# Performance work log

Measured on AMD Instinct MI355X. Metric: run time of the kernel, lower is better.

Reference implementation:

```python
import jax, jax.numpy as jnp
import numpy as np

B, IMG, P, S, D, H, HD = 64, 224, 16, 197, 768, 12, 64
MLP, L, PRUNE_AFTER, NCLS = 3072, 12, 4, 1000
N_KEEP = max(1, int(S * 0.5))  # FIXED_RATIO = 0.5 -> 98 kept tokens (plus forced CLS)


def _ln(x, w, b, eps=1e-6):
    m = x.mean(-1, keepdims=True)
    v = ((x - m) ** 2).mean(-1, keepdims=True)
    return (x - m) * jax.lax.rsqrt(v + eps) * w + b


def _block(x, ln1_w, ln1_b, qkv_w, qkv_b, proj_w, proj_b,
           ln2_w, ln2_b, fc1_w, fc1_b, fc2_w, fc2_b, key_mask=None):
    b, s, _ = x.shape
    qkv = _ln(x, ln1_w, ln1_b) @ qkv_w.T + qkv_b           # [B,S,3D]
    qkv = qkv.reshape(b, s, 3, H, HD)
    q, k, v = qkv[:, :, 0], qkv[:, :, 1], qkv[:, :, 2]     # [B,S,H,HD]
    logits = jnp.einsum('bqhd,bkhd->bhqk', q * (HD ** -0.5), k)
    if key_mask is not None:
        # masking pruned keys == varlen attention restricted to kept tokens
        logits = jnp.where(key_mask[:, None, None, :], logits, -1e9)
    attn = jax.nn.softmax(logits, axis=-1)
    out = jnp.einsum('bhqk,bkhd->bqhd', attn, v).reshape(b, s, D)
    x = x + out @ proj_w.T + proj_b
    h = _ln(x, ln2_w, ln2_b)
    h = jax.nn.gelu(h @ fc1_w.T + fc1_b, approximate=False) @ fc2_w.T + fc2_b
    return x + h


def _forward(images, patch_w, patch_b, cls_token, pos_embed,
             ln1_w, ln1_b, qkv_w, qkv_b, proj_w, proj_b,
             ln2_w, ln2_b, fc1_w, fc1_b, fc2_w, fc2_b,
             norm_w, norm_b, head_w, head_b):
    # patch embed: conv stride P == non-overlapping patch projection
    x = jax.lax.conv_general_dilated(images, patch_w, (P, P), 'VALID',
                                     dimension_numbers=('NCHW', 'OIHW', 'NCHW'))
    x = x.reshape(x.shape[0], D, -1).transpose(0, 2, 1) + patch_b       # [B,196,D]
    x = jnp.concatenate([jnp.broadcast_to(cls_token, (x.shape[0], 1, D)), x], axis=1)
    x = x + pos_embed                                                    # [B,197,D]
    for i in range(PRUNE_AFTER):
        x = _block(x, ln1_w[i], ln1_b[i], qkv_w[i], qkv_b[i], proj_w[i], proj_b[i],
                   ln2_w[i], ln2_b[i], fc1_w[i], fc1_b[i], fc2_w[i], fc2_b[i])
    # norm-score topk prune (CLS always kept), as in _threshold_prune
    scores = jnp.linalg.norm(x, axis=-1)                                 # [B,S]
    _, idx = jax.lax.top_k(scores, N_KEEP)
    mask = jnp.zeros((x.shape[0], S), bool)
    mask = mask.at[jnp.arange(x.shape[0])[:, None], idx].set(True).at[:, 0].set(True)
    # Padded-mask form of triton_pack_tokens + flash_attn_varlen: pruned tokens
    # are never attended to (masked keys) and their own outputs are unused.
    for i in range(PRUNE_AFTER, L):
        x = _block(x, ln1_w[i], ln1_b[i], qkv_w[i], qkv_b[i], proj_w[i], proj_b[i],
                   ln2_w[i], ln2_b[i], fc1_w[i], fc1_b[i], fc2_w[i], fc2_b[i],
                   key_mask=mask)
    cls = _ln(x[:, 0], norm_w, norm_b)   # packed[cu[:-1]] is always the CLS token
    return cls @ head_w.T + head_b       # [B, NCLS]


def setup_inputs():
    key = jax.random.key(0)
    ks = iter(jax.random.split(key, 32))
    def rn(shape, s=0.02):
        return jax.random.normal(next(ks), shape, jnp.float32) * s
    return {
        'images': jax.random.normal(next(ks), (B, 3, IMG, IMG), jnp.float32),
        'patch_w': rn((D, 3, P, P)), 'patch_b': jnp.zeros((D,), jnp.float32),
        'cls_token': rn((1, 1, D)), 'pos_embed': rn((1, S, D)),
        'ln1_w': jnp.ones((L, D), jnp.float32), 'ln1_b': jnp.zeros((L, D), jnp.float32),
        'qkv_w': rn((L, 3 * D, D)), 'qkv_b': jnp.zeros((L, 3 * D), jnp.float32),
        'proj_w': rn((L, D, D)), 'proj_b': jnp.zeros((L, D), jnp.float32),
        'ln2_w': jnp.ones((L, D), jnp.float32), 'ln2_b': jnp.zeros((L, D), jnp.float32),
        'fc1_w': rn((L, MLP, D)), 'fc1_b': jnp.zeros((L, MLP), jnp.float32),
        'fc2_w': rn((L, D, MLP)), 'fc2_b': jnp.zeros((L, D), jnp.float32),
        'norm_w': jnp.ones((D,), jnp.float32), 'norm_b': jnp.zeros((D,), jnp.float32),
        'head_w': rn((NCLS, D)), 'head_b': jnp.zeros((NCLS,), jnp.float32),
    }


def reference(images, patch_w, patch_b, cls_token, pos_embed,
              ln1_w, ln1_b, qkv_w, qkv_b, proj_w, proj_b,
              ln2_w, ln2_b, fc1_w, fc1_b, fc2_w, fc2_b,
              norm_w, norm_b, head_w, head_b):
    return _forward(images, patch_w, patch_b, cls_token, pos_embed,
                    ln1_w, ln1_b, qkv_w, qkv_b, proj_w, proj_b,
                    ln2_w, ln2_b, fc1_w, fc1_b, fc2_w, fc2_b,
                    norm_w, norm_b, head_w, head_b)
```

## Files before the change

kernel.cpp:

```cpp
#include <hip/hip_runtime.h>
#include <hip/hip_bf16.h>
#include <cstdint>

#define NH 12
#define SQ 197
#define DIM 768
#define HDIM 64
#define BATCH 64
#define MTOK (BATCH*SQ)
#define MLPD 3072
#define NKEEP 98
#define CSLOT 100
#define MCTOK (BATCH*CSLOT)
#define VLDF 224
#define VLDC 128

typedef __attribute__((ext_vector_type(8))) short bf16x8;
typedef __attribute__((ext_vector_type(8))) unsigned short ushort8;
typedef __attribute__((ext_vector_type(4))) float floatx4;

__device__ __forceinline__ unsigned short f2bf(float f) {
  __hip_bfloat16 h = __float2bfloat16(f);
  return reinterpret_cast<unsigned short&>(h);
}

__device__ __forceinline__ float erf_fast(float x) {
  float ax = fabsf(x);
  float t = 1.f / (1.f + 0.3275911f * ax);
  float y = t * (0.254829592f + t * (-0.284496736f + t * (1.421413741f +
            t * (-1.453152027f + t * 1.061405429f))));
  float r = 1.f - y * __expf(-ax * ax);
  return copysignf(r, x);
}

__device__ __forceinline__ void gload16(const unsigned short* g, unsigned short* l) {
  __builtin_amdgcn_global_load_lds(
      (const __attribute__((address_space(1))) void*)g,
      (__attribute__((address_space(3))) void*)l, 16, 0, 0);
}

enum { EPI_PATCH = 0, EPI_QKV = 1, EPI_RESID = 2, EPI_GELU = 3, EPI_HEAD = 4, EPI_QKVC = 5 };

template<int EPI, bool CHK>
__device__ __forceinline__ void gemm_epilogue(
    floatx4 (&acc)[4][4], int m0, int n0, int wr, int wc, int l15, int l4,
    const float* __restrict__ bias, int M, int N,
    float* __restrict__ xresid, const float* __restrict__ pos,
    unsigned short* __restrict__ obf, unsigned short* __restrict__ qb,
    unsigned short* __restrict__ kb, unsigned short* __restrict__ vb,
    float* __restrict__ ofp)
{
#pragma unroll
  for (int mr = 0; mr < 4; ++mr) {
#pragma unroll
    for (int nr = 0; nr < 4; ++nr) {
#pragma unroll
      for (int j = 0; j < 4; ++j) {
        int m = m0 + wr + mr * 16 + l4 * 4 + j;
        int n = n0 + wc + nr * 16 + l15;
        if (CHK && (m >= M || n >= N)) continue;
        float val = acc[mr][nr][j] + bias[n];
        if constexpr (EPI == EPI_PATCH) {
          int b = m / 196, p = m - b * 196;
          xresid[(size_t)(b * SQ + 1 + p) * DIM + n] = val + pos[(1 + p) * DIM + n];
        } else if constexpr (EPI == EPI_QKV || EPI == EPI_QKVC) {
          constexpr int SR = (EPI == EPI_QKV) ? SQ : CSLOT;
          constexpr int VL = (EPI == EPI_QKV) ? VLDF : VLDC;
          int part = n / DIM; int within = n - part * DIM;
          int h = within >> 6, hd = within & 63;
          int b = m / SR, s = m - b * SR;
          if (part == 0)      qb[(((size_t)(b * NH + h)) * SR + s) * HDIM + hd] = f2bf(val * 0.125f);
          else if (part == 1) kb[(((size_t)(b * NH + h)) * SR + s) * HDIM + hd] = f2bf(val);
          else                vb[(((size_t)(b * NH + h)) * HDIM + hd) * VL + s] = f2bf(val);
        } else if constexpr (EPI == EPI_RESID) {
          xresid[(size_t)m * DIM + n] += val;
        } else if constexpr (EPI == EPI_GELU) {
          float g = 0.5f * val * (1.f + erf_fast(val * 0.70710678118654752f));
          obf[(size_t)m * MLPD + n] = f2bf(g);
        } else {
          ofp[(size_t)m * 1000 + n] = val;
        }
      }
    }
  }
}

template<int EPI>
__global__ __launch_bounds__(256)
void gemm_bf(const unsigned short* __restrict__ A, int lda,
             const unsigned short* __restrict__ Wb, int ldw,
             const float* __restrict__ bias,
             int M, int N, int K,
             float* __restrict__ xresid,
             const float* __restrict__ pos,
             unsigned short* __restrict__ obf,
             unsigned short* __restrict__ qb,
             unsigned short* __restrict__ kb,
             unsigned short* __restrict__ vb,
             float* __restrict__ ofp)
{
  __shared__ unsigned short As[128 * 64];
  __shared__ unsigned short Bs[128 * 64];
  const int tid = threadIdx.x;
  const int lane = tid & 63;
  const int w = tid >> 6;
  const int wr = (w >> 1) * 64, wc = (w & 1) * 64;
  const int m0 = blockIdx.y * 128, n0 = blockIdx.x * 128;
  const int l15 = lane & 15, l4 = lane >> 4;

  const int sub = lane & 7, rsub = lane >> 3;
  const int scol = ((sub ^ rsub) << 3);
  const unsigned short* gA[4];
  const unsigned short* gB[4];
  unsigned short* lA[4];
  unsigned short* lB[4];
#pragma unroll
  for (int j = 0; j < 4; ++j) {
    int t = w * 4 + j;
    int row = t * 8 + rsub;
    int ra = m0 + row; if (ra > M - 1) ra = M - 1;
    int rb = n0 + row; if (rb > N - 1) rb = N - 1;
    gA[j] = A + (size_t)ra * lda + scol;
    gB[j] = Wb + (size_t)rb * ldw + scol;
    lA[j] = &As[t * 512];
    lB[j] = &Bs[t * 512];
  }

  floatx4 acc[4][4];
#pragma unroll
  for (int i = 0; i < 4; ++i)
#pragma unroll
    for (int j = 0; j < 4; ++j) acc[i][j] = {0.f, 0.f, 0.f, 0.f};

  for (int kt = 0; kt < K; kt += 64) {
#pragma unroll
    for (int j = 0; j < 4; ++j) {
      gload16(gA[j] + kt, lA[j]);
      gload16(gB[j] + kt, lB[j]);
    }
    __syncthreads();
#pragma unroll
    for (int kk = 0; kk < 2; ++kk) {
      bf16x8 af[4], bfr[4];
#pragma unroll
      for (int mr = 0; mr < 4; ++mr) {
        int row = wr + mr * 16 + l15;
        int cs = (kk * 4 + l4) ^ (row & 7);
        af[mr] = *(const bf16x8*)&As[row * 64 + cs * 8];
      }
#pragma unroll
      for (int nr = 0; nr < 4; ++nr) {
        int row = wc + nr * 16 + l15;
        int cs = (kk * 4 + l4) ^ (row & 7);
        bfr[nr] = *(const bf16x8*)&Bs[row * 64 + cs * 8];
      }
#pragma unroll
      for (int mr = 0; mr < 4; ++mr)
#pragma unroll
        for (int nr = 0; nr < 4; ++nr)
          acc[mr][nr] = __builtin_amdgcn_mfma_f32_16x16x32_bf16(af[mr], bfr[nr], acc[mr][nr], 0, 0, 0);
    }
    __syncthreads();
  }
  if (m0 + 128 <= M && n0 + 128 <= N)
    gemm_epilogue<EPI, false>(acc, m0, n0, wr, wc, l15, l4, bias, M, N,
                              xresid, pos, obf, qb, kb, vb, ofp);
  else
    gemm_epilogue<EPI, true>(acc, m0, n0, wr, wc, l15, l4, bias, M, N,
                             xresid, pos, obf, qb, kb, vb, ofp);
}

template<int EPI>
__global__ __launch_bounds__(256)
void gemm_f32(const unsigned short* __restrict__ A, int lda,
              const float* __restrict__ Wf, int ldw,
              const float* __restrict__ bias,
              int M, int N, int K,
              float* __restrict__ xresid,
              const float* __restrict__ pos,
              unsigned short* __restrict__ obf,
              unsigned short* __restrict__ qb,
              unsigned short* __restrict__ kb,
              unsigned short* __restrict__ vb,
              float* __restrict__ ofp)
{
  __shared__ unsigned short As[128 * 64];
  __shared__ unsigned short Bs[128 * 64];
  const int tid = threadIdx.x;
  const int lane = tid & 63;
  const int w = tid >> 6;
  const int wr = (w >> 1) * 64, wc = (w & 1) * 64;
  const int m0 = blockIdx.y * 128, n0 = blockIdx.x * 128;
  const int l15 = lane & 15, l4 = lane >> 4;

  floatx4 acc[4][4];
#pragma unroll
  for (int i = 0; i < 4; ++i)
#pragma unroll
    for (int j = 0; j < 4; ++j) acc[i][j] = {0.f, 0.f, 0.f, 0.f};

  for (int kt = 0; kt < K; kt += 64) {
#pragma unroll
    for (int i = 0; i < 4; ++i) {
      int g = tid + 256 * i;
      int row = g >> 3, c = g & 7;
      int sw = (c ^ (row & 7)) * 8;
      int ra = m0 + row; if (ra > M - 1) ra = M - 1;
      ushort8 av = *(const ushort8*)(A + (size_t)ra * lda + kt + c * 8);
      *(ushort8*)&As[row * 64 + sw] = av;
      int rb = n0 + row; if (rb > N - 1) rb = N - 1;
      const float* bs = Wf + (size_t)rb * ldw + kt + c * 8;
      float4 f0 = *(const float4*)bs;
      float4 f1 = *(const float4*)(bs + 4);
      ushort8 bv;
      bv[0] = f2bf(f0.x); bv[1] = f2bf(f0.y); bv[2] = f2bf(f0.z); bv[3] = f2bf(f0.w);
      bv[4] = f2bf(f1.x); bv[5] = f2bf(f1.y); bv[6] = f2bf(f1.z); bv[7] = f2bf(f1.w);
      *(ushort8*)&Bs[row * 64 + sw] = bv;
    }
    __syncthreads();
#pragma unroll
    for (int kk = 0; kk < 2; ++kk) {
      bf16x8 af[4], bfr[4];
#pragma unroll
      for (int mr = 0; mr < 4; ++mr) {
        int row = wr + mr * 16 + l15;
        int cs = (kk * 4 + l4) ^ (row & 7);
        af[mr] = *(const bf16x8*)&As[row * 64 + cs * 8];
      }
#pragma unroll
      for (int nr = 0; nr < 4; ++nr) {
        int row = wc + nr * 16 + l15;
        int cs = (kk * 4 + l4) ^ (row & 7);
        bfr[nr] = *(const bf16x8*)&Bs[row * 64 + cs * 8];
      }
#pragma unroll
      for (int mr = 0; mr < 4; ++mr)
#pragma unroll
        for (int nr = 0; nr < 4; ++nr)
          acc[mr][nr] = __builtin_amdgcn_mfma_f32_16x16x32_bf16(af[mr], bfr[nr], acc[mr][nr], 0, 0, 0);
    }
    __syncthreads();
  }
  if (m0 + 128 <= M && n0 + 128 <= N)
    gemm_epilogue<EPI, false>(acc, m0, n0, wr, wc, l15, l4, bias, M, N,
                              xresid, pos, obf, qb, kb, vb, ofp);
  else
    gemm_epilogue<EPI, true>(acc, m0, n0, wr, wc, l15, l4, bias, M, N,
                             xresid, pos, obf, qb, kb, vb, ofp);
}

__global__ __launch_bounds__(256)
void cvt_kernel(const float* __restrict__ src, unsigned short* __restrict__ dst, int nchunks)
{
  int i = blockIdx.x * 256 + threadIdx.x;
  if (i >= nchunks) return;
  float4 f0 = *(const float4*)(src + (size_t)i * 8);
  float4 f1 = *(const float4*)(src + (size_t)i * 8 + 4);
  ushort8 v;
  v[0] = f2bf(f0.x); v[1] = f2bf(f0.y); v[2] = f2bf(f0.z); v[3] = f2bf(f0.w);
  v[4] = f2bf(f1.x); v[5] = f2bf(f1.y); v[6] = f2bf(f1.z); v[7] = f2bf(f1.w);
  *(ushort8*)(dst + (size_t)i * 8) = v;
}

__global__ __launch_bounds__(256)
void ln_kernel(const float* __restrict__ x, long long row_stride,
               const float* __restrict__ g, const float* __restrict__ b,
               unsigned short* __restrict__ out)
{
  int row = blockIdx.x;
  const float* xr = x + (size_t)row * row_stride;
  int t = threadIdx.x;
  float v0 = xr[t], v1 = xr[t + 256], v2 = xr[t + 512];
  float s = v0 + v1 + v2, sq = v0 * v0 + v1 * v1 + v2 * v2;
  __shared__ float sb[8];
  for (int o = 32; o; o >>= 1) { s += __shfl_down(s, o); sq += __shfl_down(sq, o); }
  if ((t & 63) == 0) { sb[t >> 6] = s; sb[4 + (t >> 6)] = sq; }
  __syncthreads();
  s = sb[0] + sb[1] + sb[2] + sb[3];
  sq = sb[4] + sb[5] + sb[6] + sb[7];
  float mean = s * (1.f / 768.f);
  float var = sq * (1.f / 768.f) - mean * mean;
  float rstd = rsqrtf(var + 1e-6f);
  unsigned short* orow = out + (size_t)row * DIM;
  orow[t]       = f2bf((v0 - mean) * rstd * g[t]       + b[t]);
  orow[t + 256] = f2bf((v1 - mean) * rstd * g[t + 256] + b[t + 256]);
  orow[t + 512] = f2bf((v2 - mean) * rstd * g[t + 512] + b[t + 512]);
}

template<int NT, int SROWS, int VLD, int PSTR, bool CNT>
__global__ __launch_bounds__(256)
void attn_kernel(const unsigned short* __restrict__ qb,
                 const unsigned short* __restrict__ kb,
                 const unsigned short* __restrict__ vb,
                 const int* __restrict__ cnt,
                 unsigned short* __restrict__ outA)
{
  __shared__ unsigned short Ks[NT * 16 * 64];
  __shared__ unsigned short Ps[4][16 * PSTR];
  int bh = blockIdx.x;
  int b = bh / NH, h = bh - b * NH;
  const int tid = threadIdx.x, lane = tid & 63, w = tid >> 6;
  const int l15 = lane & 15, l4 = lane >> 4;
  const unsigned short* kbase = kb + (size_t)bh * SROWS * HDIM;
  const unsigned short* qbase = qb + (size_t)bh * SROWS * HDIM;
  const unsigned short* vbase = vb + (size_t)bh * HDIM * VLD;
  const int limit = CNT ? cnt[b] : SROWS;

  constexpr int KCH = NT * 16 * 8;
  for (int i = 0; i < (KCH + 255) / 256; ++i) {
    int gch = tid + 256 * i;
    if (gch < KCH) {
      int row = gch >> 3, c = gch & 7;
      int rs = row > SROWS - 1 ? SROWS - 1 : row;
      ushort8 kv = *(const ushort8*)(kbase + (size_t)rs * HDIM + c * 8);
      *(ushort8*)&Ks[row * 64 + ((c ^ (row & 7))) * 8] = kv;
    }
  }
  __syncthreads();

  for (int qt = w; qt < NT; qt += 4) {
    int qrow = qt * 16 + l15; if (qrow > SROWS - 1) qrow = SROWS - 1;
    bf16x8 aq0 = *(const bf16x8*)(qbase + (size_t)qrow * HDIM + l4 * 8);
    bf16x8 aq1 = *(const bf16x8*)(qbase + (size_t)qrow * HDIM + 32 + l4 * 8);

    floatx4 lg[NT];
#pragma unroll
    for (int nt = 0; nt < NT; ++nt) {
      lg[nt] = {0.f, 0.f, 0.f, 0.f};
      int row = nt * 16 + l15;
      int cs0 = (l4) ^ (row & 7);
      int cs1 = (4 + l4) ^ (row & 7);
      bf16x8 bk0 = *(const bf16x8*)&Ks[row * 64 + cs0 * 8];
      bf16x8 bk1 = *(const bf16x8*)&Ks[row * 64 + cs1 * 8];
      lg[nt] = __builtin_amdgcn_mfma_f32_16x16x32_bf16(aq0, bk0, lg[nt], 0, 0, 0);
      lg[nt] = __builtin_amdgcn_mfma_f32_16x16x32_bf16(aq1, bk1, lg[nt], 0, 0, 0);
    }
    float mx[4] = {-1e30f, -1e30f, -1e30f, -1e30f};
#pragma unroll
    for (int nt = 0; nt < NT; ++nt) {
      int col = nt * 16 + l15;
      bool valid = col < limit;
#pragma unroll
      for (int j = 0; j < 4; ++j) {
        float v = valid ? lg[nt][j] : -1e9f;
        lg[nt][j] = v;
        mx[j] = fmaxf(mx[j], v);
      }
    }
#pragma unroll
    for (int j = 0; j < 4; ++j)
      for (int o = 1; o < 16; o <<= 1) mx[j] = fmaxf(mx[j], __shfl_xor(mx[j], o));
    float sm[4] = {0.f, 0.f, 0.f, 0.f};
#pragma unroll
    for (int nt = 0; nt < NT; ++nt)
#pragma unroll
      for (int j = 0; j < 4; ++j) {
        float p = __expf(lg[nt][j] - mx[j]);
        lg[nt][j] = p;
        sm[j] += p;
      }
#pragma unroll
    for (int j = 0; j < 4; ++j) {
      for (int o = 1; o < 16; o <<= 1) sm[j] += __shfl_xor(sm[j], o);
      sm[j] = 1.f / sm[j];
    }
    unsigned short* pw = &Ps[w][0];
#pragma unroll
    for (int nt = 0; nt < NT; ++nt) {
      int col = nt * 16 + l15;
#pragma unroll
      for (int j = 0; j < 4; ++j)
        pw[(l4 * 4 + j) * PSTR + col] = f2bf(lg[nt][j]);
    }
#pragma unroll
    for (int j = 0; j < 4; ++j)
      pw[(l4 * 4 + j) * PSTR + NT * 16 + l15] = 0;
    floatx4 oacc[4];
#pragma unroll
    for (int nr = 0; nr < 4; ++nr) oacc[nr] = {0.f, 0.f, 0.f, 0.f};
#pragma unroll
    for (int ks = 0; ks < VLD / 32; ++ks) {
      bf16x8 ap = *(const bf16x8*)&pw[l15 * PSTR + ks * 32 + l4 * 8];
#pragma unroll
      for (int nr = 0; nr < 4; ++nr) {
        bf16x8 bv = *(const bf16x8*)(vbase + (size_t)(nr * 16 + l15) * VLD + ks * 32 + l4 * 8);
        oacc[nr] = __builtin_amdgcn_mfma_f32_16x16x32_bf16(ap, bv, oacc[nr], 0, 0, 0);
      }
    }
#pragma unroll
    for (int nr = 0; nr < 4; ++nr)
#pragma unroll
      for (int j = 0; j < 4; ++j) {
        int qi = qt * 16 + l4 * 4 + j;
        if (qi < SROWS)
          outA[((size_t)(b * SROWS + qi)) * DIM + h * HDIM + nr * 16 + l15] = f2bf(oacc[nr][j] * sm[j]);
      }
  }
}

__global__ __launch_bounds__(256)
void im2col_kernel(const float* __restrict__ images, unsigned short* __restrict__ out)
{
  int idx = blockIdx.x * 256 + threadIdx.x;
  int token = idx / 96;
  int kc = (idx - token * 96) * 8;
  int b = token / 196, p = token - b * 196;
  int py = p / 14, px = p - py * 14;
  int c = kc >> 8, rem = kc & 255;
  int i = rem >> 4, j0 = rem & 15;
  const float* src = images + (((size_t)(b * 3 + c) * 224 + py * 16 + i) * 224 + px * 16 + j0);
  float4 f0 = *(const float4*)src;
  float4 f1 = *(const float4*)(src + 4);
  ushort8 v;
  v[0] = f2bf(f0.x); v[1] = f2bf(f0.y); v[2] = f2bf(f0.z); v[3] = f2bf(f0.w);
  v[4] = f2bf(f1.x); v[5] = f2bf(f1.y); v[6] = f2bf(f1.z); v[7] = f2bf(f1.w);
  *(ushort8*)(out + (size_t)token * DIM + kc) = v;
}

__global__ __launch_bounds__(256)
void clspos_kernel(const float* __restrict__ cls, const float* __restrict__ pos,
                   float* __restrict__ x)
{
  int idx = blockIdx.x * 256 + threadIdx.x;
  int b = idx / DIM, d = idx - b * DIM;
  x[(size_t)(b * SQ) * DIM + d] = cls[d] + pos[d];
}

__global__ __launch_bounds__(256)
void norms_kernel(const float* __restrict__ x, float* __restrict__ norms)
{
  int row = blockIdx.x * 4 + (threadIdx.x >> 6);
  if (row >= MTOK) return;
  int lane = threadIdx.x & 63;
  const float* xr = x + (size_t)row * DIM;
  float acc = 0.f;
  for (int d = lane; d < DIM; d += 64) { float v = xr[d]; acc += v * v; }
  for (int o = 32; o; o >>= 1) acc += __shfl_down(acc, o);
  if (lane == 0) norms[row] = acc;
}

__global__ __launch_bounds__(256)
void topk_select(const float* __restrict__ norms, short* __restrict__ sidx,
                 int* __restrict__ cntg)
{
  int b = blockIdx.x;
  __shared__ float sc[SQ];
  __shared__ unsigned char keep[SQ];
  int tid = threadIdx.x;
  if (tid < SQ) sc[tid] = norms[b * SQ + tid];
  __syncthreads();
  if (tid < SQ) {
    float mine = sc[tid];
    int rank = 0;
    for (int j = 0; j < SQ; ++j) {
      float v = sc[j];
      rank += (v > mine) || (v == mine && j < tid);
    }
    keep[tid] = (rank < NKEEP) || (tid == 0);
  }
  __syncthreads();
  if (tid == 0) {
    short* row = sidx + b * CSLOT;
    int c = 0;
    for (int s = 0; s < SQ; ++s) if (keep[s]) row[c++] = (short)s;
    cntg[b] = c;
    for (int s = c; s < CSLOT; ++s) row[s] = 0;
  }
}

__global__ __launch_bounds__(192)
void gather_kernel(const float* __restrict__ x, const short* __restrict__ sidx,
                   float* __restrict__ xc)
{
  int g = blockIdx.x;
  int b = g / CSLOT;
  int src = sidx[g];
  const float4* sp = (const float4*)(x + ((size_t)(b * SQ + src)) * DIM);
  float4* dp = (float4*)(xc + (size_t)g * DIM);
  dp[threadIdx.x] = sp[threadIdx.x];
}

template<int EPI>
static inline void launch_gemm(dim3 grid, hipStream_t stream, bool usebf,
                               const unsigned short* A, int lda,
                               const float* Wf, const unsigned short* Wb, int ldw,
                               const float* bias, int M, int N, int K,
                               float* xresid, const float* pos,
                               unsigned short* obf, unsigned short* qb,
                               unsigned short* kb, unsigned short* vb, float* ofp)
{
  if (usebf)
    gemm_bf<EPI><<<grid, 256, 0, stream>>>(A, lda, Wb, ldw, bias,
        M, N, K, xresid, pos, obf, qb, kb, vb, ofp);
  else
    gemm_f32<EPI><<<grid, 256, 0, stream>>>(A, lda, Wf, ldw, bias,
        M, N, K, xresid, pos, obf, qb, kb, vb, ofp);
}

extern "C" void kernel_launch(void* const* d_in, const int* in_sizes, int n_in,
                              void* d_out, int out_size, void* d_ws, size_t ws_size,
                              hipStream_t stream)
{
  const float* images    = (const float*)d_in[0];
  const float* patch_w   = (const float*)d_in[1];
  const float* patch_b   = (const float*)d_in[2];
  const float* cls_token = (const float*)d_in[3];
  const float* pos_embed = (const float*)d_in[4];
  const float* ln1_w = (const float*)d_in[5];
  const float* ln1_b = (const float*)d_in[6];
  const float* qkv_w = (const float*)d_in[7];
  const float* qkv_b = (const float*)d_in[8];
  const float* proj_w = (const float*)d_in[9];
  const float* proj_b = (const float*)d_in[10];
  const float* ln2_w = (const float*)d_in[11];
  const float* ln2_b = (const float*)d_in[12];
  const float* fc1_w = (const float*)d_in[13];
  const float* fc1_b = (const float*)d_in[14];
  const float* fc2_w = (const float*)d_in[15];
  const float* fc2_b = (const float*)d_in[16];
  const float* norm_w = (const float*)d_in[17];
  const float* norm_b = (const float*)d_in[18];
  const float* head_w = (const float*)d_in[19];
  const float* head_b = (const float*)d_in[20];

  char* ws = (char*)d_ws;
  size_t off = 0;
  auto alloc = [&](size_t bytes) { void* p = ws + off; off += (bytes + 255) & ~(size_t)255; return p; };
  float* x            = (float*)alloc((size_t)MTOK * DIM * 4);
  float* xc           = (float*)alloc((size_t)MCTOK * DIM * 4);
  unsigned short* xn  = (unsigned short*)alloc((size_t)MTOK * DIM * 2);
  size_t h1_bytes = (size_t)MTOK * MLPD * 2;
  unsigned short* h1  = (unsigned short*)alloc(h1_bytes);
  unsigned short* qb  = h1;
  unsigned short* kb  = qb + (size_t)BATCH * NH * SQ * HDIM;
  unsigned short* vb  = kb + (size_t)BATCH * NH * SQ * HDIM;
  size_t vbytes = (size_t)BATCH * NH * HDIM * VLDF * 2;
  unsigned short* lncls = (unsigned short*)alloc((size_t)64 * DIM * 2);
  float* norms = (float*)alloc((size_t)MTOK * 4);
  short* sidx  = (short*)alloc((size_t)MCTOK * 2);
  int* cnt = (int*)alloc(BATCH * 4);
  size_t n_qkvw = (size_t)12 * 2304 * DIM, n_projw = (size_t)12 * DIM * DIM;
  size_t n_fc1w = (size_t)12 * MLPD * DIM, n_fc2w = (size_t)12 * DIM * MLPD;
  size_t n_patw = (size_t)DIM * DIM, n_headw = (size_t)1000 * DIM;
  unsigned short* wqkv = (unsigned short*)alloc(n_qkvw * 2);
  unsigned short* wproj = (unsigned short*)alloc(n_projw * 2);
  unsigned short* wfc1 = (unsigned short*)alloc(n_fc1w * 2);
  unsigned short* wfc2 = (unsigned short*)alloc(n_fc2w * 2);
  unsigned short* wpat = (unsigned short*)alloc(n_patw * 2);
  unsigned short* whead = (unsigned short*)alloc(n_headw * 2);
  const bool usebf = (off <= ws_size);

  hipMemsetAsync(vb, 0, vbytes, stream);

  if (usebf) {
    cvt_kernel<<<(int)((n_qkvw/8 + 255)/256), 256, 0, stream>>>(qkv_w, wqkv, (int)(n_qkvw/8));
    cvt_kernel<<<(int)((n_projw/8 + 255)/256), 256, 0, stream>>>(proj_w, wproj, (int)(n_projw/8));
    cvt_kernel<<<(int)((n_fc1w/8 + 255)/256), 256, 0, stream>>>(fc1_w, wfc1, (int)(n_fc1w/8));
    cvt_kernel<<<(int)((n_fc2w/8 + 255)/256), 256, 0, stream>>>(fc2_w, wfc2, (int)(n_fc2w/8));
    cvt_kernel<<<(int)((n_patw/8 + 255)/256), 256, 0, stream>>>(patch_w, wpat, (int)(n_patw/8));
    cvt_kernel<<<(int)((n_headw/8 + 255)/256), 256, 0, stream>>>(head_w, whead, (int)(n_headw/8));
  }

  im2col_kernel<<<4704, 256, 0, stream>>>(images, h1);
  launch_gemm<EPI_PATCH>(dim3(6, 98), stream, usebf, h1, DIM, patch_w, wpat, DIM,
      patch_b, 12544, DIM, DIM, x, pos_embed, nullptr, nullptr, nullptr, nullptr, nullptr);
  clspos_kernel<<<192, 256, 0, stream>>>(cls_token, pos_embed, x);

  for (int l = 0; l < 4; ++l) {
    ln_kernel<<<MTOK, 256, 0, stream>>>(x, DIM, ln1_w + l * DIM, ln1_b + l * DIM, xn);
    launch_gemm<EPI_QKV>(dim3(18, 99), stream, usebf, xn, DIM,
        qkv_w + (size_t)l * 2304 * DIM, wqkv + (size_t)l * 2304 * DIM, DIM,
        qkv_b + l * 2304, MTOK, 2304, DIM, nullptr, nullptr, nullptr, qb, kb, vb, nullptr);
    attn_kernel<13, SQ, VLDF, 248, false><<<BATCH * NH, 256, 0, stream>>>(qb, kb, vb, nullptr, xn);
    launch_gemm<EPI_RESID>(dim3(6, 99), stream, usebf, xn, DIM,
        proj_w + (size_t)l * DIM * DIM, wproj + (size_t)l * DIM * DIM, DIM,
        proj_b + l * DIM, MTOK, DIM, DIM, x, nullptr, nullptr, nullptr, nullptr, nullptr, nullptr);
    ln_kernel<<<MTOK, 256, 0, stream>>>(x, DIM, ln2_w + l * DIM, ln2_b + l * DIM, xn);
    launch_gemm<EPI_GELU>(dim3(24, 99), stream, usebf, xn, DIM,
        fc1_w + (size_t)l * MLPD * DIM, wfc1 + (size_t)l * MLPD * DIM, DIM,
        fc1_b + l * MLPD, MTOK, MLPD, DIM, nullptr, nullptr, h1, nullptr, nullptr, nullptr, nullptr);
    launch_gemm<EPI_RESID>(dim3(6, 99), stream, usebf, h1, MLPD,
        fc2_w + (size_t)l * DIM * MLPD, wfc2 + (size_t)l * DIM * MLPD, MLPD,
        fc2_b + l * DIM, MTOK, DIM, MLPD, x, nullptr, nullptr, nullptr, nullptr, nullptr, nullptr);
  }

  norms_kernel<<<(MTOK + 3) / 4, 256, 0, stream>>>(x, norms);
  topk_select<<<BATCH, 256, 0, stream>>>(norms, sidx, cnt);
  gather_kernel<<<MCTOK, 192, 0, stream>>>(x, sidx, xc);

  for (int l = 4; l < 12; ++l) {
    ln_kernel<<<MCTOK, 256, 0, stream>>>(xc, DIM, ln1_w + l * DIM, ln1_b + l * DIM, xn);
    launch_gemm<EPI_QKVC>(dim3(18, 50), stream, usebf, xn, DIM,
        qkv_w + (size_t)l * 2304 * DIM, wqkv + (size_t)l * 2304 * DIM, DIM,
        qkv_b + l * 2304, MCTOK, 2304, DIM, nullptr, nullptr, nullptr, qb, kb, vb, nullptr);
    attn_kernel<7, CSLOT, VLDC, 136, true><<<BATCH * NH, 256, 0, stream>>>(qb, kb, vb, cnt, xn);
    launch_gemm<EPI_RESID>(dim3(6, 50), stream, usebf, xn, DIM,
        proj_w + (size_t)l * DIM * DIM, wproj + (size_t)l * DIM * DIM, DIM,
        proj_b + l * DIM, MCTOK, DIM, DIM, xc, nullptr, nullptr, nullptr, nullptr, nullptr, nullptr);
    ln_kernel<<<MCTOK, 256, 0, stream>>>(xc, DIM, ln2_w + l * DIM, ln2_b + l * DIM, xn);
    launch_gemm<EPI_GELU>(dim3(24, 50), stream, usebf, xn, DIM,
        fc1_w + (size_t)l * MLPD * DIM, wfc1 + (size_t)l * MLPD * DIM, DIM,
        fc1_b + l * MLPD, MCTOK, MLPD, DIM, nullptr, nullptr, h1, nullptr, nullptr, nullptr, nullptr);
    launch_gemm<EPI_RESID>(dim3(6, 50), stream, usebf, h1, MLPD,
        fc2_w + (size_t)l * DIM * MLPD, wfc2 + (size_t)l * DIM * MLPD, MLPD,
        fc2_b + l * DIM, MCTOK, DIM, MLPD, xc, nullptr, nullptr, nullptr, nullptr, nullptr, nullptr);
  }

  ln_kernel<<<64, 256, 0, stream>>>(xc, (long long)CSLOT * DIM, norm_w, norm_b, lncls);
  launch_gemm<EPI_HEAD>(dim3(8, 1), stream, usebf, lncls, DIM, head_w, whead, DIM,
      head_b, 64, 1000, DIM, nullptr, nullptr, nullptr, nullptr, nullptr, nullptr, (float*)d_out);
  (void)in_sizes; (void)n_in; (void)out_size;
}
```

Measured before the change: 4.114 ms.

## Double-buffer LDS tiles in bf16 GEMM and remap workgroups across XCDs

New measurement: 3.848 ms. -6.5%, faster.

```diff
diff --git a/kernel.cpp b/kernel.cpp
--- a/kernel.cpp
+++ b/kernel.cpp
@@ -99,21 +99,27 @@
              unsigned short* __restrict__ vb,
              float* __restrict__ ofp)
 {
-  __shared__ unsigned short As[128 * 64];
-  __shared__ unsigned short Bs[128 * 64];
+  __shared__ unsigned short As[2][128 * 64];
+  __shared__ unsigned short Bs[2][128 * 64];
   const int tid = threadIdx.x;
   const int lane = tid & 63;
   const int w = tid >> 6;
   const int wr = (w >> 1) * 64, wc = (w & 1) * 64;
-  const int m0 = blockIdx.y * 128, n0 = blockIdx.x * 128;
+
+  const int gx = gridDim.x;
+  const int nwg = gx * gridDim.y;
+  const int orig = blockIdx.y * gx + blockIdx.x;
+  const int q = nwg >> 3, r = nwg & 7;
+  const int xcd = orig & 7, o8 = orig >> 3;
+  const int wgid = ((xcd < r) ? xcd * (q + 1) : r * (q + 1) + (xcd - r) * q) + o8;
+  const int bx = wgid % gx, by = wgid / gx;
+  const int m0 = by * 128, n0 = bx * 128;
   const int l15 = lane & 15, l4 = lane >> 4;
 
   const int sub = lane & 7, rsub = lane >> 3;
   const int scol = ((sub ^ rsub) << 3);
   const unsigned short* gA[4];
   const unsigned short* gB[4];
-  unsigned short* lA[4];
-  unsigned short* lB[4];
 #pragma unroll
   for (int j = 0; j < 4; ++j) {
     int t = w * 4 + j;
@@ -122,9 +128,18 @@
     int rb = n0 + row; if (rb > N - 1) rb = N - 1;
     gA[j] = A + (size_t)ra * lda + scol;
     gB[j] = Wb + (size_t)rb * ldw + scol;
-    lA[j] = &As[t * 512];
-    lB[j] = &Bs[t * 512];
-  }
+  }
+
+  auto STAGE = [&](int buf, int kt) {
+    unsigned short* Ad = &As[buf][0];
+    unsigned short* Bd = &Bs[buf][0];
+#pragma unroll
+    for (int j = 0; j < 4; ++j) {
+      int t = w * 4 + j;
+      gload16(gA[j] + kt, Ad + t * 512);
+      gload16(gB[j] + kt, Bd + t * 512);
+    }
+  };
 
   floatx4 acc[4][4];
 #pragma unroll
@@ -132,13 +147,20 @@
 #pragma unroll
     for (int j = 0; j < 4; ++j) acc[i][j] = {0.f, 0.f, 0.f, 0.f};
 
-  for (int kt = 0; kt < K; kt += 64) {
-#pragma unroll
-    for (int j = 0; j < 4; ++j) {
-      gload16(gA[j] + kt, lA[j]);
-      gload16(gB[j] + kt, lB[j]);
-    }
-    __syncthreads();
+  const int nk = K >> 6;
+  STAGE(0, 0);
+  int cur = 0;
+  for (int ki = 0; ki < nk; ++ki) {
+    if (ki + 1 < nk) {
+      STAGE(cur ^ 1, (ki + 1) << 6);
+      asm volatile("s_waitcnt vmcnt(8)" ::: "memory");
+    } else {
+      asm volatile("s_waitcnt vmcnt(0)" ::: "memory");
+    }
+    __builtin_amdgcn_sched_barrier(0);
+    __builtin_amdgcn_s_barrier();
+    const unsigned short* Ac = &As[cur][0];
+    const unsigned short* Bc = &Bs[cur][0];
 #pragma unroll
     for (int kk = 0; kk < 2; ++kk) {
       bf16x8 af[4], bfr[4];
@@ -146,13 +168,13 @@
       for (int mr = 0; mr < 4; ++mr) {
         int row = wr + mr * 16 + l15;
         int cs = (kk * 4 + l4) ^ (row & 7);
-        af[mr] = *(const bf16x8*)&As[row * 64 + cs * 8];
+        af[mr] = *(const bf16x8*)&Ac[row * 64 + cs * 8];
       }
 #pragma unroll
       for (int nr = 0; nr < 4; ++nr) {
         int row = wc + nr * 16 + l15;
         int cs = (kk * 4 + l4) ^ (row & 7);
-        bfr[nr] = *(const bf16x8*)&Bs[row * 64 + cs * 8];
+        bfr[nr] = *(const bf16x8*)&Bc[row * 64 + cs * 8];
       }
 #pragma unroll
       for (int mr = 0; mr < 4; ++mr)
@@ -160,7 +182,9 @@
         for (int nr = 0; nr < 4; ++nr)
           acc[mr][nr] = __builtin_amdgcn_mfma_f32_16x16x32_bf16(af[mr], bfr[nr], acc[mr][nr], 0, 0, 0);
     }
-    __syncthreads();
+    __builtin_amdgcn_sched_barrier(0);
+    __builtin_amdgcn_s_barrier();
+    cur ^= 1;
   }
   if (m0 + 128 <= M && n0 + 128 <= N)
     gemm_epilogue<EPI, false>(acc, m0, n0, wr, wc, l15, l4, bias, M, N,
```

## Add BN-templated GEMM tiles and XCD-aware workgroup remapping

Applied to the files above, without the earlier changes.

Measured after the change: 3.715 ms. -9.7%, faster.

```diff
diff --git a/kernel.cpp b/kernel.cpp
--- a/kernel.cpp
+++ b/kernel.cpp
@@ -41,9 +41,9 @@
 
 enum { EPI_PATCH = 0, EPI_QKV = 1, EPI_RESID = 2, EPI_GELU = 3, EPI_HEAD = 4, EPI_QKVC = 5 };
 
-template<int EPI, bool CHK>
+template<int EPI, bool CHK, int NR>
 __device__ __forceinline__ void gemm_epilogue(
-    floatx4 (&acc)[4][4], int m0, int n0, int wr, int wc, int l15, int l4,
+    floatx4 (&acc)[4][NR], int m0, int n0, int wr, int wc, int l15, int l4,
     const float* __restrict__ bias, int M, int N,
     float* __restrict__ xresid, const float* __restrict__ pos,
     unsigned short* __restrict__ obf, unsigned short* __restrict__ qb,
@@ -53,7 +53,7 @@
 #pragma unroll
   for (int mr = 0; mr < 4; ++mr) {
 #pragma unroll
-    for (int nr = 0; nr < 4; ++nr) {
+    for (int nr = 0; nr < NR; ++nr) {
 #pragma unroll
       for (int j = 0; j < 4; ++j) {
         int m = m0 + wr + mr * 16 + l4 * 4 + j;
@@ -85,7 +85,7 @@
   }
 }
 
-template<int EPI>
+template<int EPI, int BN>
 __global__ __launch_bounds__(256)
 void gemm_bf(const unsigned short* __restrict__ A, int lda,
              const unsigned short* __restrict__ Wb, int ldw,
@@ -99,49 +99,61 @@
              unsigned short* __restrict__ vb,
              float* __restrict__ ofp)
 {
+  constexpr int NR = BN / 32;
+  constexpr int NG = (128 + BN) / 8;
+  constexpr int PG = NG / 4;
   __shared__ unsigned short As[128 * 64];
-  __shared__ unsigned short Bs[128 * 64];
+  __shared__ unsigned short Bs[BN * 64];
   const int tid = threadIdx.x;
   const int lane = tid & 63;
   const int w = tid >> 6;
-  const int wr = (w >> 1) * 64, wc = (w & 1) * 64;
-  const int m0 = blockIdx.y * 128, n0 = blockIdx.x * 128;
+  const int wr = (w >> 1) * 64, wc = (w & 1) * (BN / 2);
+
+  const int gx = gridDim.x;
+  const int nwg = gx * gridDim.y;
+  const int orig = blockIdx.y * gx + blockIdx.x;
+  const int q = nwg >> 3, r = nwg & 7;
+  const int xcd = orig & 7, o8 = orig >> 3;
+  const int wgid = ((xcd < r) ? xcd * (q + 1) : r * (q + 1) + (xcd - r) * q) + o8;
+  const int bx = wgid % gx, by = wgid / gx;
+  const int m0 = by * 128, n0 = bx * BN;
   const int l15 = lane & 15, l4 = lane >> 4;
 
   const int sub = lane & 7, rsub = lane >> 3;
   const int scol = ((sub ^ rsub) << 3);
-  const unsigned short* gA[4];
-  const unsigned short* gB[4];
-  unsigned short* lA[4];
-  unsigned short* lB[4];
-#pragma unroll
-  for (int j = 0; j < 4; ++j) {
-    int t = w * 4 + j;
-    int row = t * 8 + rsub;
-    int ra = m0 + row; if (ra > M - 1) ra = M - 1;
-    int rb = n0 + row; if (rb > N - 1) rb = N - 1;
-    gA[j] = A + (size_t)ra * lda + scol;
-    gB[j] = Wb + (size_t)rb * ldw + scol;
-    lA[j] = &As[t * 512];
-    lB[j] = &Bs[t * 512];
-  }
-
-  floatx4 acc[4][4];
+  const unsigned short* gp[PG];
+  unsigned short* lp[PG];
+#pragma unroll
+  for (int j = 0; j < PG; ++j) {
+    int t = w * PG + j;
+    if (t < 16) {
+      int row = t * 8 + rsub;
+      int ra = m0 + row; if (ra > M - 1) ra = M - 1;
+      gp[j] = A + (size_t)ra * lda + scol;
+      lp[j] = &As[t * 512];
+    } else {
+      int tb = t - 16;
+      int row = tb * 8 + rsub;
+      int rb = n0 + row; if (rb > N - 1) rb = N - 1;
+      gp[j] = Wb + (size_t)rb * ldw + scol;
+      lp[j] = &Bs[tb * 512];
+    }
+  }
+
+  floatx4 acc[4][NR];
 #pragma unroll
   for (int i = 0; i < 4; ++i)
 #pragma unroll
-    for (int j = 0; j < 4; ++j) acc[i][j] = {0.f, 0.f, 0.f, 0.f};
+    for (int j = 0; j < NR; ++j) acc[i][j] = {0.f, 0.f, 0.f, 0.f};
 
   for (int kt = 0; kt < K; kt += 64) {
 #pragma unroll
-    for (int j = 0; j < 4; ++j) {
-      gload16(gA[j] + kt, lA[j]);
-      gload16(gB[j] + kt, lB[j]);
-    }
+    for (int j = 0; j < PG; ++j)
+      gload16(gp[j] + kt, lp[j]);
     __syncthreads();
 #pragma unroll
     for (int kk = 0; kk < 2; ++kk) {
-      bf16x8 af[4], bfr[4];
+      bf16x8 af[4], bfr[NR];
 #pragma unroll
       for (int mr = 0; mr < 4; ++mr) {
         int row = wr + mr * 16 + l15;
@@ -149,7 +161,7 @@
         af[mr] = *(const bf16x8*)&As[row * 64 + cs * 8];
       }
 #pragma unroll
-      for (int nr = 0; nr < 4; ++nr) {
+      for (int nr = 0; nr < NR; ++nr) {
         int row = wc + nr * 16 + l15;
         int cs = (kk * 4 + l4) ^ (row & 7);
         bfr[nr] = *(const bf16x8*)&Bs[row * 64 + cs * 8];
@@ -157,17 +169,17 @@
 #pragma unroll
       for (int mr = 0; mr < 4; ++mr)
 #pragma unroll
-        for (int nr = 0; nr < 4; ++nr)
+        for (int nr = 0; nr < NR; ++nr)
           acc[mr][nr] = __builtin_amdgcn_mfma_f32_16x16x32_bf16(af[mr], bfr[nr], acc[mr][nr], 0, 0, 0);
     }
     __syncthreads();
   }
-  if (m0 + 128 <= M && n0 + 128 <= N)
-    gemm_epilogue<EPI, false>(acc, m0, n0, wr, wc, l15, l4, bias, M, N,
-                              xresid, pos, obf, qb, kb, vb, ofp);
+  if (m0 + 128 <= M && n0 + BN <= N)
+    gemm_epilogue<EPI, false, NR>(acc, m0, n0, wr, wc, l15, l4, bias, M, N,
+                                  xresid, pos, obf, qb, kb, vb, ofp);
   else
-    gemm_epilogue<EPI, true>(acc, m0, n0, wr, wc, l15, l4, bias, M, N,
-                             xresid, pos, obf, qb, kb, vb, ofp);
+    gemm_epilogue<EPI, true, NR>(acc, m0, n0, wr, wc, l15, l4, bias, M, N,
+                                 xresid, pos, obf, qb, kb, vb, ofp);
 }
 
 template<int EPI>
@@ -242,11 +254,11 @@
     __syncthreads();
   }
   if (m0 + 128 <= M && n0 + 128 <= N)
-    gemm_epilogue<EPI, false>(acc, m0, n0, wr, wc, l15, l4, bias, M, N,
-                              xresid, pos, obf, qb, kb, vb, ofp);
+    gemm_epilogue<EPI, false, 4>(acc, m0, n0, wr, wc, l15, l4, bias, M, N,
+                                 xresid, pos, obf, qb, kb, vb, ofp);
   else
-    gemm_epilogue<EPI, true>(acc, m0, n0, wr, wc, l15, l4, bias, M, N,
-                             xresid, pos, obf, qb, kb, vb, ofp);
+    gemm_epilogue<EPI, true, 4>(acc, m0, n0, wr, wc, l15, l4, bias, M, N,
+                                xresid, pos, obf, qb, kb, vb, ofp);
 }
 
 __global__ __launch_bounds__(256)
@@ -480,8 +492,8 @@
   dp[threadIdx.x] = sp[threadIdx.x];
 }
 
-template<int EPI>
-static inline void launch_gemm(dim3 grid, hipStream_t stream, bool usebf,
+template<int EPI, int BN>
+static inline void launch_gemm(hipStream_t stream, bool usebf,
                                const unsigned short* A, int lda,
                                const float* Wf, const unsigned short* Wb, int ldw,
                                const float* bias, int M, int N, int K,
@@ -489,12 +501,15 @@
                                unsigned short* obf, unsigned short* qb,
                                unsigned short* kb, unsigned short* vb, float* ofp)
 {
-  if (usebf)
-    gemm_bf<EPI><<<grid, 256, 0, stream>>>(A, lda, Wb, ldw, bias,
+  if (usebf) {
+    dim3 grid((N + BN - 1) / BN, (M + 127) / 128);
+    gemm_bf<EPI, BN><<<grid, 256, 0, stream>>>(A, lda, Wb, ldw, bias,
         M, N, K, xresid, pos, obf, qb, kb, vb, ofp);
-  else
+  } else {
+    dim3 grid((N + 127) / 128, (M + 127) / 128);
     gemm_f32<EPI><<<grid, 256, 0, stream>>>(A, lda, Wf, ldw, bias,
         M, N, K, xresid, pos, obf, qb, kb, vb, ofp);
+  }
 }
 
 extern "C" void kernel_launch(void* const* d_in, const int* in_sizes, int n_in,
@@ -562,24 +577,24 @@
   }
 
   im2col_kernel<<<4704, 256, 0, stream>>>(images, h1);
-  launch_gemm<EPI_PATCH>(dim3(6, 98), stream, usebf, h1, DIM, patch_w, wpat, DIM,
+  launch_gemm<EPI_PATCH, 64>(stream, usebf, h1, DIM, patch_w, wpat, DIM,
       patch_b, 12544, DIM, DIM, x, pos_embed, nullptr, nullptr, nullptr, nullptr, nullptr);
   clspos_kernel<<<192, 256, 0, stream>>>(cls_token, pos_embed, x);
 
   for (int l = 0; l < 4; ++l) {
     ln_kernel<<<MTOK, 256, 0, stream>>>(x, DIM, ln1_w + l * DIM, ln1_b + l * DIM, xn);
-    launch_gemm<EPI_QKV>(dim3(18, 99), stream, usebf, xn, DIM,
+    launch_gemm<EPI_QKV, 128>(stream, usebf, xn, DIM,
         qkv_w + (size_t)l * 2304 * DIM, wqkv + (size_t)l * 2304 * DIM, DIM,
         qkv_b + l * 2304, MTOK, 2304, DIM, nullptr, nullptr, nullptr, qb, kb, vb, nullptr);
     attn_kernel<13, SQ, VLDF, 248, false><<<BATCH * NH, 256, 0, stream>>>(qb, kb, vb, nullptr, xn);
-    launch_gemm<EPI_RESID>(dim3(6, 99), stream, usebf, xn, DIM,
+    launch_gemm<EPI_RESID, 64>(stream, usebf, xn, DIM,
         proj_w + (size_t)l * DIM * DIM, wproj + (size_t)l * DIM * DIM, DIM,
         proj_b + l * DIM, MTOK, DIM, DIM, x, nullptr, nullptr, nullptr, nullptr, nullptr, nullptr);
     ln_kernel<<<MTOK, 256, 0, stream>>>(x, DIM, ln2_w + l * DIM, ln2_b + l * DIM, xn);
-    launch_gemm<EPI_GELU>(dim3(24, 99), stream, usebf, xn, DIM,
+    launch_gemm<EPI_GELU, 128>(stream, usebf, xn, DIM,
         fc1_w + (size_t)l * MLPD * DIM, wfc1 + (size_t)l * MLPD * DIM, DIM,
         fc1_b + l * MLPD, MTOK, MLPD, DIM, nullptr, nullptr, h1, nullptr, nullptr, nullptr, nullptr);
-    launch_gemm<EPI_RESID>(dim3(6, 99), stream, usebf, h1, MLPD,
+    launch_gemm<EPI_RESID, 64>(stream, usebf, h1, MLPD,
         fc2_w + (size_t)l * DIM * MLPD, wfc2 + (size_t)l * DIM * MLPD, MLPD,
         fc2_b + l * DIM, MTOK, DIM, MLPD, x, nullptr, nullptr, nullptr, nullptr, nullptr, nullptr);
   }
@@ -590,24 +605,24 @@
 
   for (int l = 4; l < 12; ++l) {
     ln_kernel<<<MCTOK, 256, 0, stream>>>(xc, DIM, ln1_w + l * DIM, ln1_b + l * DIM, xn);
-    launch_gemm<EPI_QKVC>(dim3(18, 50), stream, usebf, xn, DIM,
+    launch_gemm<EPI_QKVC, 128>(stream, usebf, xn, DIM,
         qkv_w + (size_t)l * 2304 * DIM, wqkv + (size_t)l * 2304 * DIM, DIM,
         qkv_b + l * 2304, MCTOK, 2304, DIM, nullptr, nullptr, nullptr, qb, kb, vb, nullptr);
     attn_kernel<7, CSLOT, VLDC, 136, true><<<BATCH * NH, 256, 0, stream>>>(qb, kb, vb, cnt, xn);
-    launch_gemm<EPI_RESID>(dim3(6, 50), stream, usebf, xn, DIM,
+    launch_gemm<EPI_RESID, 64>(stream, usebf, xn, DIM,
         proj_w + (size_t)l * DIM * DIM, wproj + (size_t)l * DIM * DIM, DIM,
         proj_b + l * DIM, MCTOK, DIM, DIM, xc, nullptr, nullptr, nullptr, nullptr, nullptr, nullptr);
     ln_kernel<<<MCTOK, 256, 0, stream>>>(xc, DIM, ln2_w + l * DIM, ln2_b + l * DIM, xn);
-    launch_gemm<EPI_GELU>(dim3(24, 50), stream, usebf, xn, DIM,
+    launch_gemm<EPI_GELU, 128>(stream, usebf, xn, DIM,
         fc1_w + (size_t)l * MLPD * DIM, wfc1 + (size_t)l * MLPD * DIM, DIM,
         fc1_b + l * MLPD, MCTOK, MLPD, DIM, nullptr, nullptr, h1, nullptr, nullptr, nullptr, nullptr);
-    launch_gemm<EPI_RESID>(dim3(6, 50), stream, usebf, h1, MLPD,
+    launch_gemm<EPI_RESID, 64>(stream, usebf, h1, MLPD,
         fc2_w + (size_t)l * DIM * MLPD, wfc2 + (size_t)l * DIM * MLPD, MLPD,
         fc2_b + l * DIM, MCTOK, DIM, MLPD, xc, nullptr, nullptr, nullptr, nullptr, nullptr, nullptr);
   }
 
   ln_kernel<<<64, 256, 0, stream>>>(xc, (long long)CSLOT * DIM, norm_w, norm_b, lncls);
-  launch_gemm<EPI_HEAD>(dim3(8, 1), stream, usebf, lncls, DIM, head_w, whead, DIM,
+  launch_gemm<EPI_HEAD, 64>(stream, usebf, lncls, DIM, head_w, whead, DIM,
       head_b, 64, 1000, DIM, nullptr, nullptr, nullptr, nullptr, nullptr, nullptr, (float*)d_out);
   (void)in_sizes; (void)n_in; (void)out_size;
 }
```
